# Optimization experiments

Measured on AMD Instinct MI355X. Metric: run time of the kernel, lower is better.

The kernel has to match this reference:

```python
import jax, jax.numpy as jnp
import numpy as np

B, F_BINS, K = 8192, 2048, 6
LS, LBW, BWMAX = 0.1, 0.05, 4.0   # lambda_sparse, lambda_bw_excess, bw_soft_max
LAP, LPK, LUM = 0.5, 0.3, 0.1     # lambda_ap, lambda_peaks, lambda_unmatched
BIG = 1e9


def _huber_mean(p, t):
    # F.huber_loss with delta=1.0, mean reduction
    e = p - t
    a = jnp.abs(e)
    return jnp.mean(jnp.where(a < 1.0, 0.5 * e * e, a - 0.5))


def _soft_match_peaks(pred_cfs, gt_cfs, gt_mask):
    """Greedy nearest-neighbour matching, sequential over the K GT slots."""
    b, k = pred_cfs.shape
    dist = jnp.abs(gt_cfs[:, :, None] - pred_cfs[:, None, :])  # [B, K_gt, K_pred]
    active = gt_mask > 0.5                                      # [B, K]

    def step(slot_used, inp):
        d_j, act_j = inp                               # [B, K], [B]
        d_m = jnp.where(slot_used, BIG, d_j)
        best = jnp.argmin(d_m, axis=1)                 # [B]
        idx = jnp.where(act_j, best, -1)
        hit = (best[:, None] == jnp.arange(k)[None, :]) & act_j[:, None]
        return slot_used | hit, idx

    used0 = jnp.zeros((b, k), dtype=bool)
    used, match_idx = jax.lax.scan(step, used0, (jnp.moveaxis(dist, 1, 0), active.T))
    matched = used.astype(pred_cfs.dtype)
    return match_idx.T, matched, 1.0 - matched  # [B,K] long, [B,K] float, [B,K] float


def _total_loss(pred_psd, true_psd, cfs, amps, bws, exponent, offset,
                gt_cfs, gt_amps, gt_bws, gt_offset, gt_exponent, peak_mask):
    # reconstruction terms
    l_recon = _huber_mean(pred_psd, true_psd)
    l_sparse = jnp.mean(amps)
    bw_excess = jnp.maximum(bws - BWMAX, 0.0)
    l_bw = jnp.mean(bw_excess * bw_excess)
    total = l_recon + LS * l_sparse + LBW * l_bw

    # supervised aperiodic term
    l_ap = jnp.mean((exponent[:, 0] - gt_exponent) ** 2) + jnp.mean((offset[:, 0] - gt_offset) ** 2)

    # matched peak terms
    match_idx, matched, unmatched = _soft_match_peaks(cfs, gt_cfs, peak_mask)
    n_real = jnp.maximum(jnp.sum(peak_mask), 1.0)
    idx = jnp.maximum(match_idx, 0)
    # torch leaves GT columns with no active entry at zero
    col_any = jnp.any(peak_mask > 0.5, axis=0)

    def gathered(v):
        return jnp.where(col_any[None, :], jnp.take_along_axis(v, idx, axis=1), 0.0)

    def masked_mse(p, t):
        return jnp.sum(((p - t) ** 2) * peak_mask) / n_real

    l_peaks = (masked_mse(gathered(cfs), gt_cfs)
               + masked_mse(gathered(amps), gt_amps)
               + masked_mse(gathered(bws), gt_bws))
    l_um = jnp.sum(amps * unmatched) / jnp.maximum(jnp.sum(unmatched), 1.0)

    return total + LAP * l_ap + LPK * l_peaks + LUM * l_um


def setup_inputs() -> dict:
    key = jax.random.key(0)
    ks = jax.random.split(key, 13)
    peak_mask = jax.random.randint(ks[7], (B, K), 0, 2).astype(jnp.float32)
    return {
        "pred_psd": jax.random.normal(ks[0], (B, F_BINS), dtype=jnp.float32),
        "true_psd": jax.random.normal(ks[1], (B, F_BINS), dtype=jnp.float32),
        "cfs": jax.random.uniform(ks[2], (B, K), minval=1.0, maxval=30.0),
        "amps": jax.random.uniform(ks[3], (B, K), minval=0.0, maxval=1.5),
        "bws": jax.random.uniform(ks[4], (B, K), minval=0.5, maxval=6.0),
        "exponent": jax.random.normal(ks[5], (B, 1), dtype=jnp.float32),
        "offset": jax.random.normal(ks[6], (B, 1), dtype=jnp.float32),
        # GT peaks: sorted ascending, zero-padded where mask==0
        "gt_cfs": jnp.sort(jax.random.uniform(ks[8], (B, K), minval=1.0, maxval=30.0), axis=1) * peak_mask,
        "gt_amps": jax.random.uniform(ks[9], (B, K), minval=0.0, maxval=1.5) * peak_mask,
        "gt_bws": jax.random.uniform(ks[10], (B, K), minval=0.5, maxval=6.0) * peak_mask,
        "gt_offset": jax.random.normal(ks[11], (B,), dtype=jnp.float32),
        "gt_exponent": jax.random.normal(ks[12], (B,), dtype=jnp.float32),
        "peak_mask": peak_mask,
    }


def reference(pred_psd, true_psd, cfs, amps, bws, exponent, offset,
              gt_cfs, gt_amps, gt_bws, gt_offset, gt_exponent, peak_mask):
    return _total_loss(pred_psd, true_psd, cfs, amps, bws, exponent, offset,
                       gt_cfs, gt_amps, gt_bws, gt_offset, gt_exponent, peak_mask)
```

## Files before the change

kernel.cpp:

```cpp
#include <hip/hip_runtime.h>

#define BATCH   8192
#define FBINS   2048
#define KSLOTS  6

#define HBLOCKS 4096
#define HTHREADS 256
#define HSTRIDE (HBLOCKS * HTHREADS)
#define HITERS  4

#define RTHREADS 256
#define RBLOCKS (BATCH / RTHREADS)
#define TOTBLOCKS (HBLOCKS + RBLOCKS)

#define LS   0.1f
#define LBW  0.05f
#define BWMAX 4.0f
#define LAP  0.5f
#define LPK  0.3f
#define LUM  0.1f

#define KEEP4(v) asm volatile("" :: "v"((v).x), "v"((v).y), "v"((v).z), "v"((v).w))

__device__ __forceinline__ float huber4(float4 a, float4 b) {
    float s = 0.f;
    { float e = a.x - b.x; float ab = fabsf(e); s += (ab < 1.f) ? 0.5f * e * e : ab - 0.5f; }
    { float e = a.y - b.y; float ab = fabsf(e); s += (ab < 1.f) ? 0.5f * e * e : ab - 0.5f; }
    { float e = a.z - b.z; float ab = fabsf(e); s += (ab < 1.f) ? 0.5f * e * e : ab - 0.5f; }
    { float e = a.w - b.w; float ab = fabsf(e); s += (ab < 1.f) ? 0.5f * e * e : ab - 0.5f; }
    return s;
}

__global__ __launch_bounds__(HTHREADS) void fused_partial(
    const float* __restrict__ pred,  const float* __restrict__ tgt,
    const float* __restrict__ cfs,   const float* __restrict__ amps,
    const float* __restrict__ bws,   const float* __restrict__ expn,
    const float* __restrict__ offs,  const float* __restrict__ gt_cfs,
    const float* __restrict__ gt_amps, const float* __restrict__ gt_bws,
    const float* __restrict__ gt_off, const float* __restrict__ gt_exp,
    const float* __restrict__ mask,
    float* __restrict__ hpart, float* __restrict__ rpart)
{
    __shared__ float sm[7][HTHREADS];

    if (blockIdx.x < HBLOCKS) {
        const int tid0 = blockIdx.x * HTHREADS + threadIdx.x;
        const float4* __restrict__ p4 = (const float4*)pred;
        const float4* __restrict__ t4 = (const float4*)tgt;

        float4 a0 = p4[tid0];
        float4 b0 = t4[tid0];
        float4 a1 = p4[tid0 + HSTRIDE];
        float4 b1 = t4[tid0 + HSTRIDE];
        float4 a2 = p4[tid0 + 2 * HSTRIDE];
        float4 b2 = t4[tid0 + 2 * HSTRIDE];
        float4 a3 = p4[tid0 + 3 * HSTRIDE];
        float4 b3 = t4[tid0 + 3 * HSTRIDE];
        KEEP4(a0); KEEP4(b0); KEEP4(a1); KEEP4(b1);
        KEEP4(a2); KEEP4(b2); KEEP4(a3); KEEP4(b3);

        float s = huber4(a0, b0);
        s += huber4(a1, b1);
        s += huber4(a2, b2);
        s += huber4(a3, b3);

        #pragma unroll
        for (int o = 32; o > 0; o >>= 1)
            s += __shfl_down(s, o, 64);

        int wave = threadIdx.x >> 6;
        int lane = threadIdx.x & 63;
        if (lane == 0) sm[0][wave] = s;
        __syncthreads();
        if (threadIdx.x == 0)
            hpart[blockIdx.x] = sm[0][0] + sm[0][1] + sm[0][2] + sm[0][3];
        return;
    }

    const int rb = blockIdx.x - HBLOCKS;
    const int b = rb * HTHREADS + threadIdx.x;

    float amps_sum = 0.f, bw_sum = 0.f, ap_sum = 0.f, peaks_sum = 0.f;
    float mask_sum = 0.f, um_cnt = 0.f, um_amps = 0.f;

    {
        float c[KSLOTS], a[KSLOTS], w[KSLOTS];
        float gc[KSLOTS], ga[KSLOTS], gw[KSLOTS], m[KSLOTS];
        #pragma unroll
        for (int i = 0; i < KSLOTS; i++) {
            c[i]  = cfs[b * KSLOTS + i];
            a[i]  = amps[b * KSLOTS + i];
            w[i]  = bws[b * KSLOTS + i];
            gc[i] = gt_cfs[b * KSLOTS + i];
            ga[i] = gt_amps[b * KSLOTS + i];
            gw[i] = gt_bws[b * KSLOTS + i];
            m[i]  = mask[b * KSLOTS + i];
        }

        bool used[KSLOTS];
        #pragma unroll
        for (int i = 0; i < KSLOTS; i++) used[i] = false;

        for (int j = 0; j < KSLOTS; j++) {
            if (m[j] > 0.5f) {
                int best = -1;
                float bd = 3.402823e+38f;
                #pragma unroll
                for (int i = 0; i < KSLOTS; i++) {
                    if (!used[i]) {
                        float d = fabsf(gc[j] - c[i]);
                        if (d < bd) { bd = d; best = i; }
                    }
                }
                used[best] = true;
                float dc = c[best] - gc[j];
                float da = a[best] - ga[j];
                float dw = w[best] - gw[j];
                peaks_sum += dc * dc + da * da + dw * dw;
                mask_sum  += 1.f;
            }
        }

        #pragma unroll
        for (int i = 0; i < KSLOTS; i++) {
            amps_sum += a[i];
            float ex = fmaxf(w[i] - BWMAX, 0.f);
            bw_sum += ex * ex;
            if (!used[i]) { um_cnt += 1.f; um_amps += a[i]; }
        }

        float de = expn[b] - gt_exp[b];
        float dof = offs[b] - gt_off[b];
        ap_sum = de * de + dof * dof;
    }

    sm[0][threadIdx.x] = amps_sum;
    sm[1][threadIdx.x] = bw_sum;
    sm[2][threadIdx.x] = ap_sum;
    sm[3][threadIdx.x] = peaks_sum;
    sm[4][threadIdx.x] = mask_sum;
    sm[5][threadIdx.x] = um_cnt;
    sm[6][threadIdx.x] = um_amps;
    __syncthreads();
    for (int o = HTHREADS / 2; o > 0; o >>= 1) {
        if (threadIdx.x < o) {
            #pragma unroll
            for (int cidx = 0; cidx < 7; cidx++)
                sm[cidx][threadIdx.x] += sm[cidx][threadIdx.x + o];
        }
        __syncthreads();
    }
    if (threadIdx.x < 7) rpart[7 * rb + threadIdx.x] = sm[threadIdx.x][0];
}

__global__ __launch_bounds__(256) void finalize(
    const float* __restrict__ hpart, const float* __restrict__ rpart,
    float* __restrict__ out)
{
    __shared__ double sm[256];
    double s = 0.0;
    #pragma unroll
    for (int r = 0; r < HBLOCKS / 256; r++)
        s += (double)hpart[r * 256 + threadIdx.x];
    sm[threadIdx.x] = s;
    __syncthreads();
    for (int o = 128; o > 0; o >>= 1) {
        if (threadIdx.x < o) sm[threadIdx.x] += sm[threadIdx.x + o];
        __syncthreads();
    }

    if (threadIdx.x == 0) {
        double huber_total = sm[0];
        double acc[7];
        for (int c = 0; c < 7; c++) acc[c] = 0.0;
        for (int blk = 0; blk < RBLOCKS; blk++)
            for (int c = 0; c < 7; c++)
                acc[c] += (double)rpart[7 * blk + c];

        double amps_sum  = acc[0];
        double bw_sum    = acc[1];
        double ap_sum    = acc[2];
        double peaks_sum = acc[3];
        double mask_sum  = acc[4];
        double um_cnt    = acc[5];
        double um_amps   = acc[6];

        double l_recon  = huber_total / ((double)BATCH * FBINS);
        double l_sparse = amps_sum / ((double)BATCH * KSLOTS);
        double l_bw     = bw_sum / ((double)BATCH * KSLOTS);
        double l_ap     = ap_sum / (double)BATCH;
        double n_real   = mask_sum > 1.0 ? mask_sum : 1.0;
        double l_peaks  = peaks_sum / n_real;
        double n_um     = um_cnt > 1.0 ? um_cnt : 1.0;
        double l_um     = um_amps / n_um;

        double total = l_recon + (double)LS * l_sparse + (double)LBW * l_bw
                     + (double)LAP * l_ap + (double)LPK * l_peaks + (double)LUM * l_um;
        out[0] = (float)total;
    }
}

extern "C" void kernel_launch(void* const* d_in, const int* in_sizes, int n_in,
                              void* d_out, int out_size, void* d_ws, size_t ws_size,
                              hipStream_t stream) {
    const float* pred_psd = (const float*)d_in[0];
    const float* true_psd = (const float*)d_in[1];
    const float* cfs      = (const float*)d_in[2];
    const float* amps     = (const float*)d_in[3];
    const float* bws      = (const float*)d_in[4];
    const float* expn     = (const float*)d_in[5];
    const float* offs     = (const float*)d_in[6];
    const float* gt_cfs   = (const float*)d_in[7];
    const float* gt_amps  = (const float*)d_in[8];
    const float* gt_bws   = (const float*)d_in[9];
    const float* gt_off   = (const float*)d_in[10];
    const float* gt_exp   = (const float*)d_in[11];
    const float* mask     = (const float*)d_in[12];
    float* out = (float*)d_out;

    float* hpart = (float*)d_ws;
    float* rpart = hpart + HBLOCKS;

    fused_partial<<<TOTBLOCKS, HTHREADS, 0, stream>>>(
        pred_psd, true_psd, cfs, amps, bws, expn, offs,
        gt_cfs, gt_amps, gt_bws, gt_off, gt_exp, mask, hpart, rpart);
    finalize<<<1, 256, 0, stream>>>(hpart, rpart, out);
}
```

Measured before the change: 33.14 us.

## Stage Huber inputs through LDS with direct global-to-LDS loads and wave-shuffle reductions

The Huber partial-sum path now uses global_load_lds to move pred/target tiles straight into shared memory, with 512-thread blocks each handling a contiguous 2048-float4 chunk instead of strided register loads. The per-sample block reduction swaps the shared-memory tree with 7 accumulators for wave shuffles plus a small cross-wave LDS step. The aim is more memory-level parallelism and fewer barriers. In exchange it uses 64 KB of LDS per block, which may limit occupancy, and it adds an extra LDS round trip for the streamed data.

New measurement: 30.98 us. 6.5% less time.

```diff
diff --git a/kernel.cpp b/kernel.cpp
--- a/kernel.cpp
+++ b/kernel.cpp
@@ -4,13 +4,14 @@
 #define FBINS   2048
 #define KSLOTS  6
 
-#define HBLOCKS 4096
-#define HTHREADS 256
-#define HSTRIDE (HBLOCKS * HTHREADS)
-#define HITERS  4
-
-#define RTHREADS 256
-#define RBLOCKS (BATCH / RTHREADS)
+#define HTHREADS 512
+#define HWAVES   (HTHREADS / 64)
+#define HBLOCKS  2048
+#define BLK_F4   2048
+#define WAVE_F4  (BLK_F4 / HWAVES)
+#define SPT      4
+
+#define RBLOCKS   (BATCH / HTHREADS)
 #define TOTBLOCKS (HBLOCKS + RBLOCKS)
 
 #define LS   0.1f
@@ -20,7 +21,11 @@
 #define LPK  0.3f
 #define LUM  0.1f
 
-#define KEEP4(v) asm volatile("" :: "v"((v).x), "v"((v).y), "v"((v).z), "v"((v).w))
+__device__ __forceinline__ void gload16(const void* g, void* l) {
+    __builtin_amdgcn_global_load_lds(
+        (const __attribute__((address_space(1))) void*)g,
+        (__attribute__((address_space(3))) void*)l, 16, 0, 0);
+}
 
 __device__ __forceinline__ float huber4(float4 a, float4 b) {
     float s = 0.f;
@@ -41,47 +46,56 @@
     const float* __restrict__ mask,
     float* __restrict__ hpart, float* __restrict__ rpart)
 {
-    __shared__ float sm[7][HTHREADS];
+    __shared__ float4 ldsA[BLK_F4];
+    __shared__ float4 ldsB[BLK_F4];
+    __shared__ float  wred[HWAVES][8];
+
+    const int tid  = threadIdx.x;
+    const int wave = tid >> 6;
+    const int lane = tid & 63;
 
     if (blockIdx.x < HBLOCKS) {
-        const int tid0 = blockIdx.x * HTHREADS + threadIdx.x;
-        const float4* __restrict__ p4 = (const float4*)pred;
-        const float4* __restrict__ t4 = (const float4*)tgt;
-
-        float4 a0 = p4[tid0];
-        float4 b0 = t4[tid0];
-        float4 a1 = p4[tid0 + HSTRIDE];
-        float4 b1 = t4[tid0 + HSTRIDE];
-        float4 a2 = p4[tid0 + 2 * HSTRIDE];
-        float4 b2 = t4[tid0 + 2 * HSTRIDE];
-        float4 a3 = p4[tid0 + 3 * HSTRIDE];
-        float4 b3 = t4[tid0 + 3 * HSTRIDE];
-        KEEP4(a0); KEEP4(b0); KEEP4(a1); KEEP4(b1);
-        KEEP4(a2); KEEP4(b2); KEEP4(a3); KEEP4(b3);
-
-        float s = huber4(a0, b0);
-        s += huber4(a1, b1);
-        s += huber4(a2, b2);
-        s += huber4(a3, b3);
+        const float4* __restrict__ a4 = (const float4*)pred;
+        const float4* __restrict__ b4 = (const float4*)tgt;
+        const int wbase = wave * WAVE_F4;
+        const long long gbase = (long long)blockIdx.x * BLK_F4 + wbase;
+
+        #pragma unroll
+        for (int s = 0; s < SPT; s++)
+            gload16(&a4[gbase + s * 64 + lane], &ldsA[wbase + s * 64]);
+        #pragma unroll
+        for (int s = 0; s < SPT; s++)
+            gload16(&b4[gbase + s * 64 + lane], &ldsB[wbase + s * 64]);
+        asm volatile("s_waitcnt vmcnt(0)" ::: "memory");
+
+        float ssum = 0.f;
+        #pragma unroll
+        for (int s = 0; s < SPT; s++) {
+            float4 a = ldsA[wbase + s * 64 + lane];
+            float4 b = ldsB[wbase + s * 64 + lane];
+            ssum += huber4(a, b);
+        }
 
         #pragma unroll
         for (int o = 32; o > 0; o >>= 1)
-            s += __shfl_down(s, o, 64);
-
-        int wave = threadIdx.x >> 6;
-        int lane = threadIdx.x & 63;
-        if (lane == 0) sm[0][wave] = s;
+            ssum += __shfl_down(ssum, o, 64);
+        if (lane == 0) wred[wave][0] = ssum;
         __syncthreads();
-        if (threadIdx.x == 0)
-            hpart[blockIdx.x] = sm[0][0] + sm[0][1] + sm[0][2] + sm[0][3];
+        if (tid == 0) {
+            float t = 0.f;
+            #pragma unroll
+            for (int w = 0; w < HWAVES; w++) t += wred[w][0];
+            hpart[blockIdx.x] = t;
+        }
         return;
     }
 
     const int rb = blockIdx.x - HBLOCKS;
-    const int b = rb * HTHREADS + threadIdx.x;
-
-    float amps_sum = 0.f, bw_sum = 0.f, ap_sum = 0.f, peaks_sum = 0.f;
-    float mask_sum = 0.f, um_cnt = 0.f, um_amps = 0.f;
+    const int b = rb * HTHREADS + tid;
+
+    float acc[7];
+    #pragma unroll
+    for (int c = 0; c < 7; c++) acc[c] = 0.f;
 
     {
         float c[KSLOTS], a[KSLOTS], w[KSLOTS];
@@ -116,41 +130,43 @@
                 float dc = c[best] - gc[j];
                 float da = a[best] - ga[j];
                 float dw = w[best] - gw[j];
-                peaks_sum += dc * dc + da * da + dw * dw;
-                mask_sum  += 1.f;
+                acc[3] += dc * dc + da * da + dw * dw;
+                acc[4] += 1.f;
             }
         }
 
         #pragma unroll
         for (int i = 0; i < KSLOTS; i++) {
-            amps_sum += a[i];
+            acc[0] += a[i];
             float ex = fmaxf(w[i] - BWMAX, 0.f);
-            bw_sum += ex * ex;
-            if (!used[i]) { um_cnt += 1.f; um_amps += a[i]; }
+            acc[1] += ex * ex;
+            if (!used[i]) { acc[5] += 1.f; acc[6] += a[i]; }
         }
 
         float de = expn[b] - gt_exp[b];
         float dof = offs[b] - gt_off[b];
-        ap_sum = de * de + dof * dof;
-    }
-
-    sm[0][threadIdx.x] = amps_sum;
-    sm[1][threadIdx.x] = bw_sum;
-    sm[2][threadIdx.x] = ap_sum;
-    sm[3][threadIdx.x] = peaks_sum;
-    sm[4][threadIdx.x] = mask_sum;
-    sm[5][threadIdx.x] = um_cnt;
-    sm[6][threadIdx.x] = um_amps;
+        acc[2] = de * de + dof * dof;
+    }
+
+    #pragma unroll
+    for (int c = 0; c < 7; c++) {
+        float v = acc[c];
+        #pragma unroll
+        for (int o = 32; o > 0; o >>= 1)
+            v += __shfl_down(v, o, 64);
+        acc[c] = v;
+    }
+    if (lane == 0) {
+        #pragma unroll
+        for (int c = 0; c < 7; c++) wred[wave][c] = acc[c];
+    }
     __syncthreads();
-    for (int o = HTHREADS / 2; o > 0; o >>= 1) {
-        if (threadIdx.x < o) {
-            #pragma unroll
-            for (int cidx = 0; cidx < 7; cidx++)
-                sm[cidx][threadIdx.x] += sm[cidx][threadIdx.x + o];
-        }
-        __syncthreads();
-    }
-    if (threadIdx.x < 7) rpart[7 * rb + threadIdx.x] = sm[threadIdx.x][0];
+    if (tid < 7) {
+        float t = 0.f;
+        #pragma unroll
+        for (int w = 0; w < HWAVES; w++) t += wred[w][tid];
+        rpart[7 * rb + tid] = t;
+    }
 }
 
 __global__ __launch_bounds__(256) void finalize(
@@ -177,22 +193,14 @@
             for (int c = 0; c < 7; c++)
                 acc[c] += (double)rpart[7 * blk + c];
 
-        double amps_sum  = acc[0];
-        double bw_sum    = acc[1];
-        double ap_sum    = acc[2];
-        double peaks_sum = acc[3];
-        double mask_sum  = acc[4];
-        double um_cnt    = acc[5];
-        double um_amps   = acc[6];
-
         double l_recon  = huber_total / ((double)BATCH * FBINS);
-        double l_sparse = amps_sum / ((double)BATCH * KSLOTS);
-        double l_bw     = bw_sum / ((double)BATCH * KSLOTS);
-        double l_ap     = ap_sum / (double)BATCH;
-        double n_real   = mask_sum > 1.0 ? mask_sum : 1.0;
-        double l_peaks  = peaks_sum / n_real;
-        double n_um     = um_cnt > 1.0 ? um_cnt : 1.0;
-        double l_um     = um_amps / n_um;
+        double l_sparse = acc[0] / ((double)BATCH * KSLOTS);
+        double l_bw     = acc[1] / ((double)BATCH * KSLOTS);
+        double l_ap     = acc[2] / (double)BATCH;
+        double n_real   = acc[4] > 1.0 ? acc[4] : 1.0;
+        double l_peaks  = acc[3] / n_real;
+        double n_um     = acc[5] > 1.0 ? acc[5] : 1.0;
+        double l_um     = acc[6] / n_um;
 
         double total = l_recon + (double)LS * l_sparse + (double)LBW * l_bw
                      + (double)LAP * l_ap + (double)LPK * l_peaks + (double)LUM * l_um;
```
